# Kernel optimization log

Hardware: AMD Instinct MI355X
Metric: run time of the kernel (lower is better)

Reference implementation:

```python
import jax, jax.numpy as jnp
import numpy as np

TOKENS, INDIM, OUTDIM = 8192, 4096, 4096


def setup_inputs() -> dict:
    key = jax.random.key(0)
    k1, k2, k3 = jax.random.split(key, 3)
    x = jax.random.normal(k1, (TOKENS, INDIM), dtype=jnp.float32)
    # xavier_uniform for weight (outdim, indim)
    limit = float(np.sqrt(6.0 / (INDIM + OUTDIM)))
    weight = jax.random.uniform(k2, (OUTDIM, INDIM), dtype=jnp.float32,
                                minval=-limit, maxval=limit)
    bias = jnp.zeros((OUTDIM,), dtype=jnp.float32)
    # expander-graph style 0/1 mask at density ~0.5 (static buffer)
    mask = jax.random.randint(k3, (OUTDIM, INDIM), 0, 2, dtype=jnp.int32)
    return {"x": x, "weight": weight, "bias": bias, "mask": mask}


def reference(x, weight, bias, mask):
    # ExpanderLinearFunction: y = x @ (weight * mask)^T + bias
    w_masked = weight * mask.astype(weight.dtype)  # [outdim, indim]
    return jnp.einsum('ti,oi->to', x, w_masked) + bias
```

## Files before the change

### kernel.cpp

```cpp
#include <hip/hip_runtime.h>
#include <hip/hip_bf16.h>
#include <stdint.h>


typedef __attribute__((ext_vector_type(4))) float f32x4;
typedef __attribute__((ext_vector_type(4))) int   i32x4;

static constexpr int M = 8192;
static constexpr int N = 4096;
static constexpr int K = 4096;
static constexpr int NT = K / 64;

#define GLOBAL_AS(p) ((const __attribute__((address_space(1))) void*)(p))
#define LDS_AS(p)    ((__attribute__((address_space(3))) void*)(p))

__global__ void __launch_bounds__(256)
quant_x(const float* __restrict__ x, signed char* __restrict__ xq,
        float* __restrict__ sx) {
    const int row = blockIdx.x, tid = threadIdx.x;
    const f32x4* xr = (const f32x4*)(x + (size_t)row * K);
    f32x4 v[4];
    float am = 0.0f;
#pragma unroll
    for (int c = 0; c < 4; ++c) {
        v[c] = xr[c * 256 + tid];
        am = fmaxf(am, fmaxf(fmaxf(fabsf(v[c].x), fabsf(v[c].y)),
                             fmaxf(fabsf(v[c].z), fabsf(v[c].w))));
    }
#pragma unroll
    for (int off = 32; off; off >>= 1) am = fmaxf(am, __shfl_xor(am, off));
    __shared__ float red[4];
    if ((tid & 63) == 0) red[tid >> 6] = am;
    __syncthreads();
    am = fmaxf(fmaxf(red[0], red[1]), fmaxf(red[2], red[3]));
    const float inv = am > 0.0f ? 127.0f / am : 0.0f;
    int* out = (int*)xq + (size_t)row * (K / 4);
#pragma unroll
    for (int c = 0; c < 4; ++c) {
        int q0 = (int)__builtin_rintf(v[c].x * inv) & 255;
        int q1 = (int)__builtin_rintf(v[c].y * inv) & 255;
        int q2 = (int)__builtin_rintf(v[c].z * inv) & 255;
        int q3 = (int)__builtin_rintf(v[c].w * inv) & 255;
        out[c * 256 + tid] = q0 | (q1 << 8) | (q2 << 16) | (q3 << 24);
    }
    if (tid == 0) sx[row] = am * (1.0f / 127.0f);
}

__global__ void __launch_bounds__(256)
quant_w(const float* __restrict__ w, const int* __restrict__ mask,
        signed char* __restrict__ wq, float* __restrict__ sw) {
    const int row = blockIdx.x, tid = threadIdx.x;
    const f32x4* wr = (const f32x4*)(w + (size_t)row * K);
    const i32x4* mr = (const i32x4*)(mask + (size_t)row * K);
    f32x4 v[4];
    float am = 0.0f;
#pragma unroll
    for (int c = 0; c < 4; ++c) {
        f32x4 wv = wr[c * 256 + tid];
        i32x4 mv = mr[c * 256 + tid];
        v[c].x = mv.x ? wv.x : 0.0f;
        v[c].y = mv.y ? wv.y : 0.0f;
        v[c].z = mv.z ? wv.z : 0.0f;
        v[c].w = mv.w ? wv.w : 0.0f;
        am = fmaxf(am, fmaxf(fmaxf(fabsf(v[c].x), fabsf(v[c].y)),
                             fmaxf(fabsf(v[c].z), fabsf(v[c].w))));
    }
#pragma unroll
    for (int off = 32; off; off >>= 1) am = fmaxf(am, __shfl_xor(am, off));
    __shared__ float red[4];
    if ((tid & 63) == 0) red[tid >> 6] = am;
    __syncthreads();
    am = fmaxf(fmaxf(red[0], red[1]), fmaxf(red[2], red[3]));
    const float inv = am > 0.0f ? 127.0f / am : 0.0f;
    int* out = (int*)wq + (size_t)row * (K / 4);
#pragma unroll
    for (int c = 0; c < 4; ++c) {
        int q0 = (int)__builtin_rintf(v[c].x * inv) & 255;
        int q1 = (int)__builtin_rintf(v[c].y * inv) & 255;
        int q2 = (int)__builtin_rintf(v[c].z * inv) & 255;
        int q3 = (int)__builtin_rintf(v[c].w * inv) & 255;
        out[c * 256 + tid] = q0 | (q1 << 8) | (q2 << 16) | (q3 << 24);
    }
    if (tid == 0) sw[row] = am * (1.0f / 127.0f);
}

__global__ void __launch_bounds__(512, 2)
gemmI8(const signed char* __restrict__ A,
       const signed char* __restrict__ B,
       const float* __restrict__ sx,
       const float* __restrict__ sw,
       const float* __restrict__ bias,
       float* __restrict__ C) {
    extern __shared__ unsigned char lds[];
    unsigned char* __restrict__ Au = lds;
    unsigned char* __restrict__ Bu = lds + 32768;

    const int tid  = threadIdx.x;
    const int lane = tid & 63;
    const int wave = tid >> 6;

    const int bid = blockIdx.x;
    const int swz = (bid & 7) * 64 + (bid >> 3);
    const int brow = (swz >> 4) * 256;
    const int bcol = (swz & 15) * 256;

    const int wrow = (wave >> 2) * 128;
    const int wcol = (wave & 3) * 64;
    const int fr = lane & 15;
    const int fq = lane >> 4;

    const int s3r   = (((fr & 1) << 2) | fq) ^ (fr >> 1);
    const int abase = wrow * 64 + (fr >> 1) * 128 + s3r * 16;
    const int bbase = wcol * 64 + (fr >> 1) * 128 + s3r * 16;

    const int l8 = lane & 7, lh = lane >> 3;
    const int s3w    = l8 ^ lh;
    const int wrow_l = 2 * lh + (s3w >> 2);
    const int wcol_b = (s3w & 3) * 16;

    const signed char* __restrict__ Ag = A + (size_t)brow * K;
    const signed char* __restrict__ Bg = B + (size_t)bcol * K;

    i32x4 acc[8][4];
#pragma unroll
    for (int m = 0; m < 8; ++m)
#pragma unroll
        for (int n = 0; n < 4; ++n) acc[m][n] = (i32x4)(0);

    i32x4 afL[4], afH[4], bfv[4];

#define STG1(dst, src) __builtin_amdgcn_global_load_lds(GLOBAL_AS(src), LDS_AS(dst), 16, 0, 0)
#define STGA(slot, j) do {                                                      \
    _Pragma("unroll")                                                           \
    for (int c = 0; c < 2; ++c) {                                               \
        const int q_ = c * 8 + wave;                                            \
        STG1(Au + (slot) * 16384 + q_ * 1024,                                   \
             Ag + (size_t)(q_ * 16 + wrow_l) * K + (j) * 64 + wcol_b);          \
    }                                                                           \
  } while (0)
#define STGB(slot, j) do {                                                      \
    _Pragma("unroll")                                                           \
    for (int c = 0; c < 2; ++c) {                                               \
        const int q_ = c * 8 + wave;                                            \
        STG1(Bu + (slot) * 16384 + q_ * 1024,                                   \
             Bg + (size_t)(q_ * 16 + wrow_l) * K + (j) * 64 + wcol_b);          \
    }                                                                           \
  } while (0)
#define LDA4(buf, unit, m0) do {                                                \
    const unsigned char* ub_ = Au + (unit) * 16384;                             \
    _Pragma("unroll")                                                           \
    for (int i = 0; i < 4; ++i)                                                 \
        buf[i] = *(const i32x4*)(ub_ + abase + ((m0) + i) * 1024);              \
  } while (0)
#define LDB4(buf, unit) do {                                                    \
    const unsigned char* vb_ = Bu + (unit) * 16384;                             \
    _Pragma("unroll")                                                           \
    for (int n = 0; n < 4; ++n)                                                 \
        buf[n] = *(const i32x4*)(vb_ + bbase + n * 1024);                       \
  } while (0)
#define MM16(a, r0) do {                                                        \
    __builtin_amdgcn_s_setprio(1);                                              \
    _Pragma("unroll")                                                           \
    for (int i = 0; i < 4; ++i)                                                 \
      _Pragma("unroll")                                                         \
      for (int n = 0; n < 4; ++n)                                               \
        acc[(r0) + i][n] = __builtin_amdgcn_mfma_i32_16x16x64_i8(               \
            a[i], bfv[n], acc[(r0) + i][n], 0, 0, 0);                           \
    __builtin_amdgcn_s_setprio(0);                                              \
  } while (0)
#define BAR    __builtin_amdgcn_s_barrier()
#define FENCE  asm volatile("" ::: "memory")
#define WVM0   asm volatile("s_waitcnt vmcnt(0)" ::: "memory")

    STGA(0, 0); STGB(0, 0);
    WVM0;
    BAR; FENCE;

#pragma unroll 1
    for (int t = 0; t < NT; ++t) {
        const int s  = t & 1;
        const int s1 = s ^ 1;
        if (t + 1 < NT) { STGA(s1, t + 1); STGB(s1, t + 1); }
        LDA4(afL, s, 0); LDB4(bfv, s);
        BAR; FENCE;
        MM16(afL, 0);
        BAR; FENCE;
        LDA4(afH, s, 4);
        BAR; FENCE;
        MM16(afH, 4);
        WVM0;
        BAR; FENCE;
    }

    float swv[4], bvv[4];
#pragma unroll
    for (int n = 0; n < 4; ++n) {
        const int col = bcol + wcol + n * 16 + fr;
        swv[n] = sw[col];
        bvv[n] = bias[col];
    }
#pragma unroll
    for (int m = 0; m < 8; ++m) {
#pragma unroll
        for (int j = 0; j < 4; ++j) {
            const int row = brow + wrow + m * 16 + fq * 4 + j;
            const float sxr = sx[row];
            float* crow = C + (size_t)row * N + bcol + wcol + fr;
#pragma unroll
            for (int n = 0; n < 4; ++n)
                crow[n * 16] = (float)acc[m][n][j] * (sxr * swv[n]) + bvv[n];
        }
    }
#undef STG1
#undef STGA
#undef STGB
#undef LDA4
#undef LDB4
#undef MM16
#undef BAR
#undef FENCE
#undef WVM0
}

__global__ void fallback_gemm(const float* __restrict__ x,
                              const float* __restrict__ w,
                              const int* __restrict__ mask,
                              const float* __restrict__ bias,
                              float* __restrict__ C) {
    const int tid = threadIdx.x;
    const int tx = tid & 15, ty = tid >> 4;
    const int brow = blockIdx.y * 64, bcol = blockIdx.x * 64;
    __shared__ float As[64][17];
    __shared__ float Ws[64][17];
    float acc[4][4] = {};
    for (int k0 = 0; k0 < K; k0 += 16) {
        __syncthreads();
        for (int i = tid; i < 64 * 16; i += 256) {
            int r = i >> 4, c = i & 15;
            As[r][c] = x[(size_t)(brow + r) * K + k0 + c];
            float wv = w[(size_t)(bcol + r) * K + k0 + c];
            Ws[r][c] = mask[(size_t)(bcol + r) * K + k0 + c] ? wv : 0.0f;
        }
        __syncthreads();
        for (int kk = 0; kk < 16; ++kk) {
            float a[4], b[4];
#pragma unroll
            for (int i = 0; i < 4; ++i) a[i] = As[ty * 4 + i][kk];
#pragma unroll
            for (int i = 0; i < 4; ++i) b[i] = Ws[tx * 4 + i][kk];
#pragma unroll
            for (int i = 0; i < 4; ++i)
#pragma unroll
                for (int j = 0; j < 4; ++j) acc[i][j] += a[i] * b[j];
        }
    }
    for (int i = 0; i < 4; ++i)
        for (int j = 0; j < 4; ++j) {
            int row = brow + ty * 4 + i, col = bcol + tx * 4 + j;
            C[(size_t)row * N + col] = acc[i][j] + bias[col];
        }
}

extern "C" void kernel_launch(void* const* d_in, const int* in_sizes, int n_in,
                              void* d_out, int out_size, void* d_ws, size_t ws_size,
                              hipStream_t stream) {
    const float* x    = (const float*)d_in[0];
    const float* w    = (const float*)d_in[1];
    const float* bias = (const float*)d_in[2];
    const int*   mask = (const int*)d_in[3];
    float* out = (float*)d_out;

    const size_t xq_b = (size_t)M * K;
    const size_t wq_b = (size_t)N * K;
    const size_t need = xq_b + wq_b + (M + N) * sizeof(float);
    if (ws_size >= need) {
        signed char* xq = (signed char*)d_ws;
        signed char* wq = xq + xq_b;
        float* sx = (float*)(wq + wq_b);
        float* sw = sx + M;
        (void)hipFuncSetAttribute((const void*)gemmI8,
                                  hipFuncAttributeMaxDynamicSharedMemorySize,
                                  65536);
        quant_x<<<M, 256, 0, stream>>>(x, xq, sx);
        quant_w<<<N, 256, 0, stream>>>(w, mask, wq, sw);
        gemmI8<<<(M / 256) * (N / 256), 512, 65536, stream>>>(
            xq, wq, sx, sw, bias, out);
    } else {
        dim3 g(N / 64, M / 64);
        fallback_gemm<<<g, 256, 0, stream>>>(x, w, mask, bias, out);
    }
}
```

Before: 207.0 us.

## Pre-swizzle quantized weights into MFMA fragment layout and load B directly to registers

The weight quantizer now writes int8 weights in a fragment-ordered layout so each lane can load its MFMA B operand straight from global memory into registers. This bypasses LDS staging for B. The A tile now uses a four-slot LDS ring with the loop unrolled by two, and the B fragments are double-buffered in registers with partial vmcnt waits. The aim is less LDS traffic and fewer barriers per K step, at the cost of global-load latency on B, which must be hidden by the register prefetch, and more register pressure.

```diff
diff --git a/kernel.cpp b/kernel.cpp
--- a/kernel.cpp
+++ b/kernel.cpp
@@ -48,16 +48,15 @@
 
 __global__ void __launch_bounds__(256)
 quant_w(const float* __restrict__ w, const int* __restrict__ mask,
-        signed char* __restrict__ wq, float* __restrict__ sw) {
+        signed char* __restrict__ wqf, float* __restrict__ sw) {
     const int row = blockIdx.x, tid = threadIdx.x;
-    const f32x4* wr = (const f32x4*)(w + (size_t)row * K);
-    const i32x4* mr = (const i32x4*)(mask + (size_t)row * K);
+    const size_t base = (size_t)row * K + (size_t)tid * 16;
     f32x4 v[4];
     float am = 0.0f;
 #pragma unroll
     for (int c = 0; c < 4; ++c) {
-        f32x4 wv = wr[c * 256 + tid];
-        i32x4 mv = mr[c * 256 + tid];
+        f32x4 wv = *(const f32x4*)(w + base + c * 4);
+        i32x4 mv = *(const i32x4*)(mask + base + c * 4);
         v[c].x = mv.x ? wv.x : 0.0f;
         v[c].y = mv.y ? wv.y : 0.0f;
         v[c].z = mv.z ? wv.z : 0.0f;
@@ -72,28 +71,30 @@
     __syncthreads();
     am = fmaxf(fmaxf(red[0], red[1]), fmaxf(red[2], red[3]));
     const float inv = am > 0.0f ? 127.0f / am : 0.0f;
-    int* out = (int*)wq + (size_t)row * (K / 4);
+    i32x4 q;
 #pragma unroll
     for (int c = 0; c < 4; ++c) {
         int q0 = (int)__builtin_rintf(v[c].x * inv) & 255;
         int q1 = (int)__builtin_rintf(v[c].y * inv) & 255;
         int q2 = (int)__builtin_rintf(v[c].z * inv) & 255;
         int q3 = (int)__builtin_rintf(v[c].w * inv) & 255;
-        out[c * 256 + tid] = q0 | (q1 << 8) | (q2 << 16) | (q3 << 24);
-    }
+        q[c] = q0 | (q1 << 8) | (q2 << 16) | (q3 << 24);
+    }
+    const size_t off16 = ((size_t)(row >> 4) * 64 + (tid >> 2)) * 64
+                         + (size_t)(tid & 3) * 16 + (row & 15);
+    ((i32x4*)wqf)[off16] = q;
     if (tid == 0) sw[row] = am * (1.0f / 127.0f);
 }
 
 __global__ void __launch_bounds__(512, 2)
 gemmI8(const signed char* __restrict__ A,
-       const signed char* __restrict__ B,
+       const signed char* __restrict__ Bf,
        const float* __restrict__ sx,
        const float* __restrict__ sw,
        const float* __restrict__ bias,
        float* __restrict__ C) {
     extern __shared__ unsigned char lds[];
     unsigned char* __restrict__ Au = lds;
-    unsigned char* __restrict__ Bu = lds + 32768;
 
     const int tid  = threadIdx.x;
     const int lane = tid & 63;
@@ -111,7 +112,6 @@
 
     const int s3r   = (((fr & 1) << 2) | fq) ^ (fr >> 1);
     const int abase = wrow * 64 + (fr >> 1) * 128 + s3r * 16;
-    const int bbase = wcol * 64 + (fr >> 1) * 128 + s3r * 16;
 
     const int l8 = lane & 7, lh = lane >> 3;
     const int s3w    = l8 ^ lh;
@@ -119,7 +119,8 @@
     const int wcol_b = (s3w & 3) * 16;
 
     const signed char* __restrict__ Ag = A + (size_t)brow * K;
-    const signed char* __restrict__ Bg = B + (size_t)bcol * K;
+    const int SB0 = (bcol + wcol) >> 4;
+    const signed char* __restrict__ Bg = Bf + (size_t)SB0 * 65536 + lane * 16;
 
     i32x4 acc[8][4];
 #pragma unroll
@@ -127,7 +128,7 @@
 #pragma unroll
         for (int n = 0; n < 4; ++n) acc[m][n] = (i32x4)(0);
 
-    i32x4 afL[4], afH[4], bfv[4];
+    i32x4 afL[4], afH[4], bA[4], bB[4];
 
 #define STG1(dst, src) __builtin_amdgcn_global_load_lds(GLOBAL_AS(src), LDS_AS(dst), 16, 0, 0)
 #define STGA(slot, j) do {                                                      \
@@ -138,13 +139,10 @@
              Ag + (size_t)(q_ * 16 + wrow_l) * K + (j) * 64 + wcol_b);          \
     }                                                                           \
   } while (0)
-#define STGB(slot, j) do {                                                      \
-    _Pragma("unroll")                                                           \
-    for (int c = 0; c < 2; ++c) {                                               \
-        const int q_ = c * 8 + wave;                                            \
-        STG1(Bu + (slot) * 16384 + q_ * 1024,                                   \
-             Bg + (size_t)(q_ * 16 + wrow_l) * K + (j) * 64 + wcol_b);          \
-    }                                                                           \
+#define BPRE(buf, t_) do {                                                      \
+    _Pragma("unroll")                                                           \
+    for (int n = 0; n < 4; ++n)                                                 \
+        buf[n] = *(const i32x4*)(Bg + (size_t)n * 65536 + (t_) * 1024);         \
   } while (0)
 #define LDA4(buf, unit, m0) do {                                                \
     const unsigned char* ub_ = Au + (unit) * 16384;                             \
@@ -152,44 +150,53 @@
     for (int i = 0; i < 4; ++i)                                                 \
         buf[i] = *(const i32x4*)(ub_ + abase + ((m0) + i) * 1024);              \
   } while (0)
-#define LDB4(buf, unit) do {                                                    \
-    const unsigned char* vb_ = Bu + (unit) * 16384;                             \
-    _Pragma("unroll")                                                           \
-    for (int n = 0; n < 4; ++n)                                                 \
-        buf[n] = *(const i32x4*)(vb_ + bbase + n * 1024);                       \
-  } while (0)
-#define MM16(a, r0) do {                                                        \
+#define MM16(a, b, r0) do {                                                     \
     __builtin_amdgcn_s_setprio(1);                                              \
     _Pragma("unroll")                                                           \
     for (int i = 0; i < 4; ++i)                                                 \
       _Pragma("unroll")                                                         \
       for (int n = 0; n < 4; ++n)                                               \
         acc[(r0) + i][n] = __builtin_amdgcn_mfma_i32_16x16x64_i8(               \
-            a[i], bfv[n], acc[(r0) + i][n], 0, 0, 0);                           \
+            a[i], b[n], acc[(r0) + i][n], 0, 0, 0);                             \
     __builtin_amdgcn_s_setprio(0);                                              \
   } while (0)
 #define BAR    __builtin_amdgcn_s_barrier()
 #define FENCE  asm volatile("" ::: "memory")
+#define WVM2   asm volatile("s_waitcnt vmcnt(2)" ::: "memory")
 #define WVM0   asm volatile("s_waitcnt vmcnt(0)" ::: "memory")
 
-    STGA(0, 0); STGB(0, 0);
+    STGA(0, 0); STGA(1, 1);
+    BPRE(bA, 0);
     WVM0;
     BAR; FENCE;
 
 #pragma unroll 1
-    for (int t = 0; t < NT; ++t) {
-        const int s  = t & 1;
-        const int s1 = s ^ 1;
-        if (t + 1 < NT) { STGA(s1, t + 1); STGB(s1, t + 1); }
-        LDA4(afL, s, 0); LDB4(bfv, s);
-        BAR; FENCE;
-        MM16(afL, 0);
-        BAR; FENCE;
-        LDA4(afH, s, 4);
-        BAR; FENCE;
-        MM16(afH, 4);
+    for (int t = 0; t < NT - 2; t += 2) {
+        BPRE(bB, t + 1);
+        STGA((t + 2) & 3, t + 2);
+        LDA4(afL, t & 3, 0); LDA4(afH, t & 3, 4);
+        BAR; FENCE;
+        MM16(afL, bA, 0); MM16(afH, bA, 4);
+        WVM2;
+        BAR; FENCE;
+        BPRE(bA, t + 2);
+        STGA((t + 3) & 3, t + 3);
+        LDA4(afL, (t + 1) & 3, 0); LDA4(afH, (t + 1) & 3, 4);
+        BAR; FENCE;
+        MM16(afL, bB, 0); MM16(afH, bB, 4);
+        WVM2;
+        BAR; FENCE;
+    }
+    {
+        BPRE(bB, NT - 1);
+        LDA4(afL, (NT - 2) & 3, 0); LDA4(afH, (NT - 2) & 3, 4);
+        BAR; FENCE;
+        MM16(afL, bA, 0); MM16(afH, bA, 4);
         WVM0;
         BAR; FENCE;
+        LDA4(afL, (NT - 1) & 3, 0); LDA4(afH, (NT - 1) & 3, 4);
+        FENCE;
+        MM16(afL, bB, 0); MM16(afH, bB, 4);
     }
 
     float swv[4], bvv[4];
@@ -213,12 +220,12 @@
     }
 #undef STG1
 #undef STGA
-#undef STGB
+#undef BPRE
 #undef LDA4
-#undef LDB4
 #undef MM16
 #undef BAR
 #undef FENCE
+#undef WVM2
 #undef WVM0
 }
 
@@ -274,17 +281,17 @@
     const size_t wq_b = (size_t)N * K;
     const size_t need = xq_b + wq_b + (M + N) * sizeof(float);
     if (ws_size >= need) {
-        signed char* xq = (signed char*)d_ws;
-        signed char* wq = xq + xq_b;
-        float* sx = (float*)(wq + wq_b);
+        signed char* xq  = (signed char*)d_ws;
+        signed char* wqf = xq + xq_b;
+        float* sx = (float*)(wqf + wq_b);
         float* sw = sx + M;
         (void)hipFuncSetAttribute((const void*)gemmI8,
                                   hipFuncAttributeMaxDynamicSharedMemorySize,
                                   65536);
         quant_x<<<M, 256, 0, stream>>>(x, xq, sx);
-        quant_w<<<N, 256, 0, stream>>>(w, mask, wq, sw);
+        quant_w<<<N, 256, 0, stream>>>(w, mask, wqf, sw);
         gemmI8<<<(M / 256) * (N / 256), 512, 65536, stream>>>(
-            xq, wq, sx, sw, bias, out);
+            xq, wqf, sx, sw, bias, out);
     } else {
         dim3 g(N / 64, M / 64);
         fallback_gemm<<<g, 256, 0, stream>>>(x, w, mask, bias, out);
```

Result: slower. 225.7 us (+9.0%).

## Deepen int8 GEMM pipeline to four LDS stages with register double-buffering

Applied to the files above, without the earlier changes.

Moves the int8 MFMA GEMM from a 2-stage LDS ring to a 4-stage ring of 128 KB, with global loads issued two tiles ahead. The main loop is restructured into alternating phases that overlap LDS fragment reads and global-to-LDS copies with MFMA work, using double-buffered B fragments and a partial vmcnt wait. The goal is to hide global-load latency and cut barrier stalls. The cost is double the LDS per block, which likely drops occupancy from 2 blocks/CU to 1, and the s_setprio hints are removed.

```diff
diff --git a/kernel.cpp b/kernel.cpp
--- a/kernel.cpp
+++ b/kernel.cpp
@@ -93,7 +93,7 @@
        float* __restrict__ C) {
     extern __shared__ unsigned char lds[];
     unsigned char* __restrict__ Au = lds;
-    unsigned char* __restrict__ Bu = lds + 32768;
+    unsigned char* __restrict__ Bu = lds + 65536;
 
     const int tid  = threadIdx.x;
     const int lane = tid & 63;
@@ -127,18 +127,16 @@
 #pragma unroll
         for (int n = 0; n < 4; ++n) acc[m][n] = (i32x4)(0);
 
-    i32x4 afL[4], afH[4], bfv[4];
+    i32x4 A0[4], A1[4], B0[4], B1[4];
 
 #define STG1(dst, src) __builtin_amdgcn_global_load_lds(GLOBAL_AS(src), LDS_AS(dst), 16, 0, 0)
-#define STGA(slot, j) do {                                                      \
+#define SAB(slot, j) do {                                                       \
     _Pragma("unroll")                                                           \
     for (int c = 0; c < 2; ++c) {                                               \
         const int q_ = c * 8 + wave;                                            \
         STG1(Au + (slot) * 16384 + q_ * 1024,                                   \
              Ag + (size_t)(q_ * 16 + wrow_l) * K + (j) * 64 + wcol_b);          \
     }                                                                           \
-  } while (0)
-#define STGB(slot, j) do {                                                      \
     _Pragma("unroll")                                                           \
     for (int c = 0; c < 2; ++c) {                                               \
         const int q_ = c * 8 + wave;                                            \
@@ -158,39 +156,71 @@
     for (int n = 0; n < 4; ++n)                                                 \
         buf[n] = *(const i32x4*)(vb_ + bbase + n * 1024);                       \
   } while (0)
-#define MM16(a, r0) do {                                                        \
-    __builtin_amdgcn_s_setprio(1);                                              \
+#define MM16(a, b, r0) do {                                                     \
     _Pragma("unroll")                                                           \
     for (int i = 0; i < 4; ++i)                                                 \
       _Pragma("unroll")                                                         \
       for (int n = 0; n < 4; ++n)                                               \
         acc[(r0) + i][n] = __builtin_amdgcn_mfma_i32_16x16x64_i8(               \
-            a[i], bfv[n], acc[(r0) + i][n], 0, 0, 0);                           \
-    __builtin_amdgcn_s_setprio(0);                                              \
+            a[i], b[n], acc[(r0) + i][n], 0, 0, 0);                             \
   } while (0)
 #define BAR    __builtin_amdgcn_s_barrier()
 #define FENCE  asm volatile("" ::: "memory")
+#define SCHED0 __builtin_amdgcn_sched_barrier(0)
+#define WVM4   asm volatile("s_waitcnt vmcnt(4)" ::: "memory")
 #define WVM0   asm volatile("s_waitcnt vmcnt(0)" ::: "memory")
 
-    STGA(0, 0); STGB(0, 0);
-    WVM0;
+#define PHA(ut, s2, j2, bc) do {                                                \
+    BAR; FENCE;                                                                 \
+    LDA4(A1, ut, 4);                                                            \
+    SAB(s2, j2);                                                                \
+    SCHED0;                                                                     \
+    MM16(A0, bc, 0);                                                            \
+  } while (0)
+#define PHA_NOST(ut, bc) do {                                                   \
+    BAR; FENCE;                                                                 \
+    LDA4(A1, ut, 4);                                                            \
+    SCHED0;                                                                     \
+    MM16(A0, bc, 0);                                                            \
+  } while (0)
+#define PHB(un, bn, bc) do {                                                    \
+    WVM4; BAR; FENCE;                                                           \
+    LDA4(A0, un, 0);                                                            \
+    LDB4(bn, un);                                                               \
+    SCHED0;                                                                     \
+    MM16(A1, bc, 4);                                                            \
+  } while (0)
+#define PHB0(un, bn, bc) do {                                                   \
+    WVM0; BAR; FENCE;                                                           \
+    LDA4(A0, un, 0);                                                            \
+    LDB4(bn, un);                                                               \
+    SCHED0;                                                                     \
+    MM16(A1, bc, 4);                                                            \
+  } while (0)
+
+    SAB(0, 0); SAB(1, 1);
+    WVM4;
     BAR; FENCE;
+    LDA4(A0, 0, 0); LDB4(B0, 0);
 
 #pragma unroll 1
-    for (int t = 0; t < NT; ++t) {
-        const int s  = t & 1;
-        const int s1 = s ^ 1;
-        if (t + 1 < NT) { STGA(s1, t + 1); STGB(s1, t + 1); }
-        LDA4(afL, s, 0); LDB4(bfv, s);
-        BAR; FENCE;
-        MM16(afL, 0);
-        BAR; FENCE;
-        LDA4(afH, s, 4);
-        BAR; FENCE;
-        MM16(afH, 4);
-        WVM0;
-        BAR; FENCE;
-    }
+    for (int t = 0; t < NT - 4; t += 2) {
+        const int u0 = t & 3, u1 = (t + 1) & 3;
+        const int s2 = (t + 2) & 3, s3 = (t + 3) & 3;
+        PHA(u0, s2, t + 2, B0);
+        PHB(u1, B1, B0);
+        PHA(u1, s3, t + 3, B1);
+        PHB(s2, B0, B1);
+    }
+    PHA(0, 2, 62, B0);
+    PHB(1, B1, B0);
+    PHA(1, 3, 63, B1);
+    PHB(2, B0, B1);
+    PHA_NOST(2, B0);
+    PHB0(3, B1, B0);
+    PHA_NOST(3, B1);
+    FENCE;
+    MM16(A1, B1, 4);
 
     float swv[4], bvv[4];
 #pragma unroll
@@ -212,14 +242,19 @@
         }
     }
 #undef STG1
-#undef STGA
-#undef STGB
+#undef SAB
 #undef LDA4
 #undef LDB4
 #undef MM16
 #undef BAR
 #undef FENCE
+#undef SCHED0
+#undef WVM4
 #undef WVM0
+#undef PHA
+#undef PHA_NOST
+#undef PHB
+#undef PHB0
 }
 
 __global__ void fallback_gemm(const float* __restrict__ x,
@@ -280,10 +315,10 @@
         float* sw = sx + M;
         (void)hipFuncSetAttribute((const void*)gemmI8,
                                   hipFuncAttributeMaxDynamicSharedMemorySize,
-                                  65536);
+                                  131072);
         quant_x<<<M, 256, 0, stream>>>(x, xq, sx);
         quant_w<<<N, 256, 0, stream>>>(w, mask, wq, sw);
-        gemmI8<<<(M / 256) * (N / 256), 512, 65536, stream>>>(
+        gemmI8<<<(M / 256) * (N / 256), 512, 131072, stream>>>(
             xq, wq, sx, sw, bias, out);
     } else {
         dim3 g(N / 64, M / 64);
```

Measured after the change: 197.1 us. 4.8% less time.
